# Kernel tuning notes

Hardware: AMD Instinct MI355X
Metric: run time of the kernel (lower is better)

## Reference

```python
import jax, jax.numpy as jnp
import numpy as np

V, E, H = 32000, 512, 512
B, T = 64, 512


def lstm_dir(x, W, U, b, reverse=False):
    """Keras-semantics LSTM over [B,T,D] -> (hs [B,T,H], h_last, c_last).
    Gate order i,f,g,o; sigmoid recurrent activation, tanh activation.
    Inference mode: dropout=0.1 is inactive (Keras applies it only in training)."""
    xz = jnp.einsum('btd,dg->btg', x, W) + b  # precompute input projections [B,T,4H]
    if reverse:
        xz = xz[:, ::-1]
    h0 = jnp.zeros((x.shape[0], U.shape[0]), x.dtype)
    c0 = jnp.zeros_like(h0)

    def step(carry, zt):
        h, c = carry
        z = zt + h @ U
        i, f, g, o = jnp.split(z, 4, axis=-1)
        c = jax.nn.sigmoid(f) * c + jax.nn.sigmoid(i) * jnp.tanh(g)
        h = jax.nn.sigmoid(o) * jnp.tanh(c)
        return (h, c), h

    (h_last, c_last), hs = jax.lax.scan(step, (h0, c0), jnp.swapaxes(xz, 0, 1))
    hs = jnp.swapaxes(hs, 0, 1)  # [B,T,H]
    if reverse:
        hs = hs[:, ::-1]  # Keras Bidirectional re-aligns backward outputs in time
    return hs, h_last, c_last


def setup_inputs() -> dict:
    key = jax.random.key(0)
    ks = jax.random.split(key, 14)
    s = lambda fan_in: 1.0 / np.sqrt(fan_in)
    p = {
        'encoderinput': jax.random.randint(ks[0], (B, T), 0, V, dtype=jnp.int32),
        'emb': jax.random.normal(ks[1], (V, E), jnp.float32) * 0.02,
        # layer 1 (input dim E), forward and backward directions
        'W1f': jax.random.normal(ks[2], (E, 4 * H), jnp.float32) * s(E),
        'U1f': jax.random.normal(ks[3], (H, 4 * H), jnp.float32) * s(H),
        'b1f': jnp.zeros((4 * H,), jnp.float32),
        'W1b': jax.random.normal(ks[4], (E, 4 * H), jnp.float32) * s(E),
        'U1b': jax.random.normal(ks[5], (H, 4 * H), jnp.float32) * s(H),
        'b1b': jnp.zeros((4 * H,), jnp.float32),
        # layer 2 (input dim 2H from bidirectional concat)
        'W2f': jax.random.normal(ks[6], (2 * H, 4 * H), jnp.float32) * s(2 * H),
        'U2f': jax.random.normal(ks[7], (H, 4 * H), jnp.float32) * s(H),
        'b2f': jnp.zeros((4 * H,), jnp.float32),
        'W2b': jax.random.normal(ks[8], (2 * H, 4 * H), jnp.float32) * s(2 * H),
        'U2b': jax.random.normal(ks[9], (H, 4 * H), jnp.float32) * s(H),
        'b2b': jnp.zeros((4 * H,), jnp.float32),
    }
    return p


def reference(encoderinput, emb, W1f, U1f, b1f, W1b, U1b, b1b,
              W2f, U2f, b2f, W2b, U2b, b2b):
    x = emb[encoderinput]  # [B,T,E]
    hf1, _, _ = lstm_dir(x, W1f, U1f, b1f, reverse=False)
    hb1, _, _ = lstm_dir(x, W1b, U1b, b1b, reverse=True)
    l1 = jnp.concatenate([hf1, hb1], axis=-1)  # [B,T,2H]
    hf2, fh, fc = lstm_dir(l1, W2f, U2f, b2f, reverse=False)
    hb2, bh, bc = lstm_dir(l1, W2b, U2b, b2b, reverse=True)
    encoder_output = jnp.concatenate([hf2, hb2], axis=-1)  # [B,T,2H]
    state_h = jnp.concatenate([fh, bh], axis=-1)  # [B,2H]
    state_c = jnp.concatenate([fc, bc], axis=-1)  # [B,2H]
    return (encoder_output, state_h, state_c)
```

## Files before the change

kernel.cpp:

```cpp
#include <hip/hip_runtime.h>
#include <math.h>


#define NBLK_LSTM 256

typedef __attribute__((ext_vector_type(8))) short bf16x8;
typedef __attribute__((ext_vector_type(16))) float f32x16;

__device__ __forceinline__ float bf2f(unsigned short u) {
  return __uint_as_float(((unsigned)u) << 16);
}
__device__ __forceinline__ unsigned short f2bf(float f) {
  unsigned u = __float_as_uint(f);
  unsigned r = (u + 0x7FFFu + ((u >> 16) & 1u)) >> 16;
  return (unsigned short)r;
}
__device__ __forceinline__ float fsigmoid(float x) {
  return 1.0f / (1.0f + __expf(-x));
}
__device__ __forceinline__ float ftanh(float x) {
  return 1.0f - 2.0f / (1.0f + __expf(2.0f * x));
}
__device__ __forceinline__ void gload16(const void* g, void* l) {
  __builtin_amdgcn_global_load_lds(
      (const __attribute__((address_space(1))) unsigned int*)g,
      (__attribute__((address_space(3))) unsigned int*)l, 16, 0, 0);
}

__global__ __launch_bounds__(256) void transpose_u(const float* __restrict__ U,
                                                   float* __restrict__ Ut) {
  __shared__ float tile[32][33];
  int kt = blockIdx.x & 15;
  int ct = blockIdx.x >> 4;
  int k0 = kt * 32, c0 = ct * 32;
  int tx = threadIdx.x & 31, ty = threadIdx.x >> 5;
#pragma unroll
  for (int i = 0; i < 32; i += 8)
    tile[ty + i][tx] = U[(size_t)(k0 + ty + i) * 2048 + c0 + tx];
  __syncthreads();
#pragma unroll
  for (int i = 0; i < 32; i += 8)
    Ut[(size_t)(c0 + ty + i) * 512 + k0 + tx] = tile[tx][ty + i];
}

__global__ __launch_bounds__(256) void build_w_panels(
    const float* __restrict__ W, unsigned short* __restrict__ Wh,
    unsigned short* __restrict__ Wl, int KT) {
  __shared__ float tile[32][33];
  const int tid = threadIdx.x;
  int kt = blockIdx.x % KT;
  int ct = blockIdx.x / KT;
  int k0 = kt * 32, c0 = ct * 32;
  int tx = tid & 31, ty = tid >> 5;
#pragma unroll
  for (int i = 0; i < 32; i += 8)
    tile[ty + i][tx] = W[(size_t)(k0 + ty + i) * 2048 + c0 + tx];
  __syncthreads();
  const int t = tid & 127;
  const int cl = t & 31, g = t >> 5;
  const int c = c0 + cl;
  const int rm = c & 127, nt = c >> 7;
  const int slot = g ^ (rm & 3);
  size_t off = (((size_t)(nt * KT + kt) * 128 + rm) << 5) + slot * 8;
  bf16x8 hh, ll;
#pragma unroll
  for (int e = 0; e < 8; e++) {
    float f = tile[g * 8 + e][cl];
    unsigned short h = f2bf(f);
    hh[e] = (short)h;
    ll[e] = (short)f2bf(f - bf2f(h));
  }
  if (tid < 128) *(bf16x8*)(Wh + off) = hh;
  else           *(bf16x8*)(Wl + off) = ll;
}

__global__ __launch_bounds__(256) void build_a1_panels(
    const int* __restrict__ ids, const float* __restrict__ emb,
    unsigned short* __restrict__ Apan) {
  const int tid = threadIdx.x;
  const int l = tid & 63, wv = tid >> 6;
  const int m = blockIdx.x * 4 + wv;
  const float* src = emb + (size_t)ids[m] * 512 + l * 8;
  float4 v0 = *(const float4*)src;
  float4 v1 = *(const float4*)(src + 4);
  float f[8] = {v0.x, v0.y, v0.z, v0.w, v1.x, v1.y, v1.z, v1.w};
  bf16x8 hh;
#pragma unroll
  for (int e = 0; e < 8; e++) hh[e] = (short)f2bf(f[e]);
  const int rm = m & 127, mt = m >> 7;
  const int kt = l >> 2, g = l & 3;
  const int slot = g ^ (rm & 3);
  *(bf16x8*)(Apan + (((size_t)(mt * 16 + kt) * 128 + rm) << 5) + slot * 8) = hh;
}

template <int KT, int TERMS>
__global__ __launch_bounds__(256) void gemm_panel(
    const unsigned short* __restrict__ Apan,
    const unsigned short* __restrict__ WhF,
    const unsigned short* __restrict__ WlF,
    const unsigned short* __restrict__ WhB,
    const unsigned short* __restrict__ WlB,
    const float* __restrict__ bF, const float* __restrict__ bB,
    unsigned short* __restrict__ CF, unsigned short* __restrict__ CB) {
  __shared__ __align__(16) char lds[2][24576];

  const int tid = threadIdx.x;
  const int half = blockIdx.x >> 12;
  const int inner = blockIdx.x & 4095;
  const int mt = inner & 255;
  const int nt = inner >> 8;
  const int l = tid & 63;
  const int wv = tid >> 6;
  const int wm = wv >> 1, wn = wv & 1;

  const unsigned short* WhP = half ? WhB : WhF;
  const unsigned short* WlP = half ? WlB : WlF;
  const float* bias = half ? bB : bF;
  unsigned short* C = half ? CB : CF;

  const char* aSrc = (const char*)(Apan + (size_t)mt * KT * 4096);
  const char* hSrc = (const char*)(WhP + (size_t)nt * KT * 4096);
  const char* lSrc = (const char*)(WlP + (size_t)nt * KT * 4096);
  const int wvo = wv * 1024;
  const int lo16 = l * 16;

  f32x16 acc[2][2];
#pragma unroll
  for (int rb = 0; rb < 2; rb++)
#pragma unroll
    for (int cb = 0; cb < 2; cb++)
#pragma unroll
      for (int r = 0; r < 16; r++) acc[rb][cb][r] = 0.0f;

  auto STAGE = [&](int buf, int t) {
    const char* ga = aSrc + (size_t)t * 8192 + wvo + lo16;
    const char* gh = hSrc + (size_t)t * 8192 + wvo + lo16;
    char* da = &lds[buf][0] + wvo;
    char* dh = &lds[buf][8192] + wvo;
    gload16(ga, da);
    gload16(ga + 4096, da + 4096);
    gload16(gh, dh);
    gload16(gh + 4096, dh + 4096);
    if (TERMS == 2) {
      const char* gl = lSrc + (size_t)t * 8192 + wvo + lo16;
      char* dl = &lds[buf][16384] + wvo;
      gload16(gl, dl);
      gload16(gl + 4096, dl + 4096);
    }
  };

  STAGE(0, 0);
  asm volatile("s_waitcnt vmcnt(0)" ::: "memory");
  __syncthreads();

  const int aoff0 = (wm * 64 + (l & 31)) * 64;
  const int woff0 = 8192 + (wn * 64 + (l & 31)) * 64;
  const int gbase = l >> 5;
  const int gx = l & 3;

  for (int t = 0; t < KT; t++) {
    if (t + 1 < KT) STAGE((t + 1) & 1, t + 1);
    const char* lb = lds[t & 1];
#pragma unroll
    for (int ks = 0; ks < 2; ks++) {
      const int slot = (((ks << 1) + gbase) ^ gx) << 4;
      bf16x8 a0 = *(const bf16x8*)(lb + aoff0 + slot);
      bf16x8 a1 = *(const bf16x8*)(lb + aoff0 + 2048 + slot);
      bf16x8 h0 = *(const bf16x8*)(lb + woff0 + slot);
      bf16x8 h1 = *(const bf16x8*)(lb + woff0 + 2048 + slot);
      acc[0][0] = __builtin_amdgcn_mfma_f32_32x32x16_bf16(a0, h0, acc[0][0], 0, 0, 0);
      acc[0][1] = __builtin_amdgcn_mfma_f32_32x32x16_bf16(a0, h1, acc[0][1], 0, 0, 0);
      acc[1][0] = __builtin_amdgcn_mfma_f32_32x32x16_bf16(a1, h0, acc[1][0], 0, 0, 0);
      acc[1][1] = __builtin_amdgcn_mfma_f32_32x32x16_bf16(a1, h1, acc[1][1], 0, 0, 0);
      if (TERMS == 2) {
        bf16x8 w0 = *(const bf16x8*)(lb + woff0 + 8192 + slot);
        bf16x8 w1 = *(const bf16x8*)(lb + woff0 + 8192 + 2048 + slot);
        acc[0][0] = __builtin_amdgcn_mfma_f32_32x32x16_bf16(a0, w0, acc[0][0], 0, 0, 0);
        acc[0][1] = __builtin_amdgcn_mfma_f32_32x32x16_bf16(a0, w1, acc[0][1], 0, 0, 0);
        acc[1][0] = __builtin_amdgcn_mfma_f32_32x32x16_bf16(a1, w0, acc[1][0], 0, 0, 0);
        acc[1][1] = __builtin_amdgcn_mfma_f32_32x32x16_bf16(a1, w1, acc[1][1], 0, 0, 0);
      }
    }
    asm volatile("s_waitcnt vmcnt(0)" ::: "memory");
    __syncthreads();
  }

  const int m0 = mt * 128, n0 = nt * 128;
  const float b0 = bias[n0 + wn * 64 + (l & 31)];
  const float b1 = bias[n0 + wn * 64 + 32 + (l & 31)];
#pragma unroll
  for (int rb = 0; rb < 2; rb++) {
    const int rowb = m0 + wm * 64 + rb * 32 + 4 * (l >> 5);
#pragma unroll
    for (int cb = 0; cb < 2; cb++) {
      const int col = n0 + wn * 64 + cb * 32 + (l & 31);
      const float bb = cb ? b1 : b0;
#pragma unroll
      for (int r = 0; r < 16; r++) {
        const int row = rowb + (r & 3) + 8 * (r >> 2);
        C[(size_t)row * 2048 + col] = f2bf(acc[rb][cb][r] + bb);
      }
    }
  }
}

__global__ __launch_bounds__(256, 1) void lstm_fused(
    const unsigned short* __restrict__ xzF,
    const unsigned short* __restrict__ xzB,
    const float* __restrict__ UtF,
    const float* __restrict__ UtB,
    float* __restrict__ outF32,
    unsigned short* __restrict__ outB16,
    float* __restrict__ hbuf,
    float* __restrict__ stateh, float* __restrict__ statec,
    unsigned* __restrict__ bar) {
  __shared__ float p_lds[2][4][32][36];

  const int tid = threadIdx.x;
  const int bid = blockIdx.x;
  const int dir = bid >> 7;
  const int jg  = (bid & 127) >> 1;
  const int bg  = bid & 1;
  const int grp = dir * 2 + bg;

  const unsigned short* xz = dir ? xzB : xzF;
  const float* Ut = dir ? UtB : UtF;
  char* hbuf_c = (char*)hbuf;

  const int l  = tid & 63;
  const int wv = tid >> 6;

  bf16x8 uh8[8], ul8[8];
  {
    const int c = l & 31;
    const size_t gcol = (size_t)((c >> 3) * 512 + jg * 8 + (c & 7));
#pragma unroll
    for (int ks = 0; ks < 8; ks++) {
      const float* src = Ut + gcol * 512 + (wv * 8 + ks) * 16 + ((l >> 5) << 3);
      bf16x8 hh, ll;
#pragma unroll
      for (int e = 0; e < 8; e++) {
        float f = src[e];
        unsigned short us = f2bf(f);
        hh[e] = (short)us;
        ll[e] = (short)f2bf(f - bf2f(us));
      }
      uh8[ks] = hh;
      ul8[ks] = ll;
    }
  }

  const int ub = tid >> 3;
  const int jl = tid & 7;
  const int b  = bg * 32 + ub;
  const int j  = jg * 8 + jl;

  unsigned* leafArr = bar + grp * 128;
  unsigned* arriveLeaf = leafArr + ((jg >> 3) << 4);
  const unsigned* pollLeaf = leafArr + ((l & 7) << 4);

  const unsigned short* xzb = xz + (size_t)b * (512 * 2048) + j;

  float creg = 0.0f;
  float zx0, zx1, zx2, zx3;
  {
    const unsigned short* p = xzb + (size_t)(dir ? 511 : 0) * 2048;
    zx0 = bf2f(p[0]); zx1 = bf2f(p[512]);
    zx2 = bf2f(p[1024]); zx3 = bf2f(p[1536]);
  }

  const int aoff = ((wv * 16 + (l >> 5)) * 32 + (l & 31)) * 16;
  const int poff = jg * 512 + ub * 16 + jl * 2;

  const int colp = dir * 512 + j;
  const int p_kt = colp >> 5, p_g = (colp >> 3) & 3, p_e = colp & 7;

  for (int s = 0; s < 512; s++) {
    const int tt = dir ? (511 - s) : s;

    if (s > 0) {
      {
        const unsigned tgt = 32u * (unsigned)s;
        while (true) {
          unsigned v = __hip_atomic_load(pollLeaf, __ATOMIC_RELAXED,
                                         __HIP_MEMORY_SCOPE_AGENT);
          if (__all((int)(v >= tgt))) break;
          __builtin_amdgcn_s_sleep(1);
        }
      }
      const char* sb = hbuf_c + (size_t)(grp * 2 + (s & 1)) * 65536;
      bf16x8 ahh[8], ahl[8];
#pragma unroll
      for (int ks = 0; ks < 8; ks++) {
        const char* p = sb + aoff + ks * 1024;
        asm volatile("global_load_dwordx4 %0, %1, off sc0 sc1"
                     : "=v"(ahh[ks]) : "v"(p) : "memory");
      }
#pragma unroll
      for (int ks = 0; ks < 8; ks++) {
        const char* p = sb + aoff + ks * 1024 + 32768;
        asm volatile("global_load_dwordx4 %0, %1, off sc0 sc1"
                     : "=v"(ahl[ks]) : "v"(p) : "memory");
      }
      f32x16 acc;
#pragma unroll
      for (int r = 0; r < 16; r++) acc[r] = 0.0f;
      asm volatile("s_waitcnt vmcnt(8)" ::: "memory");
      __builtin_amdgcn_sched_barrier(0);
#pragma unroll
      for (int ks = 0; ks < 8; ks++)
        acc = __builtin_amdgcn_mfma_f32_32x32x16_bf16(ahh[ks], uh8[ks], acc, 0, 0, 0);
      asm volatile("s_waitcnt vmcnt(0)" ::: "memory");
      __builtin_amdgcn_sched_barrier(0);
#pragma unroll
      for (int ks = 0; ks < 8; ks++) {
        acc = __builtin_amdgcn_mfma_f32_32x32x16_bf16(ahl[ks], uh8[ks], acc, 0, 0, 0);
        acc = __builtin_amdgcn_mfma_f32_32x32x16_bf16(ahh[ks], ul8[ks], acc, 0, 0, 0);
      }
#pragma unroll
      for (int r = 0; r < 16; r++) {
        const int row = (r & 3) + 8 * (r >> 2) + 4 * (l >> 5);
        p_lds[s & 1][wv][row][l & 31] = acc[r];
      }
    }
    __syncthreads();

    float h;
    {
      float z0 = zx0, z1 = zx1, z2 = zx2, z3 = zx3;
      if (s > 0) {
#pragma unroll
        for (int w = 0; w < 4; w++) {
          z0 += p_lds[s & 1][w][ub][jl];
          z1 += p_lds[s & 1][w][ub][8 + jl];
          z2 += p_lds[s & 1][w][ub][16 + jl];
          z3 += p_lds[s & 1][w][ub][24 + jl];
        }
      }
      float si = fsigmoid(z0);
      float sf = fsigmoid(z1);
      float tg = ftanh(z2);
      float so = fsigmoid(z3);
      creg = fmaf(sf, creg, si * tg);
      h = so * ftanh(creg);
    }

    const int m = b * 512 + tt;
    if (s < 511) {
      unsigned short hhs = f2bf(h);
      unsigned short hls = f2bf(h - bf2f(hhs));
      char* db = hbuf_c + (size_t)(grp * 2 + ((s & 1) ^ 1)) * 65536;
      char* pj = db + poff;
      unsigned vh = hhs, vl = hls;
      asm volatile("global_store_short %0, %1, off sc0 sc1"
                   :: "v"(pj), "v"(vh) : "memory");
      asm volatile("global_store_short %0, %1, off sc0 sc1"
                   :: "v"(pj + 32768), "v"(vl) : "memory");
      if (outB16) {
        const int rm = m & 127, mt = m >> 7;
        outB16[(((size_t)(mt * 32 + p_kt) * 128 + rm) << 5) +
               (p_g ^ (rm & 3)) * 8 + p_e] = f2bf(h);
      } else {
        outF32[((size_t)m) * 1024 + colp] = h;
      }
      asm volatile("s_waitcnt vmcnt(0)" ::: "memory");
      if ((tid & 63) == 0)
        __hip_atomic_fetch_add(arriveLeaf, 1u, __ATOMIC_RELAXED,
                               __HIP_MEMORY_SCOPE_AGENT);
      {
        const int tn = dir ? (510 - s) : (s + 1);
        const unsigned short* p = xzb + (size_t)tn * 2048;
        zx0 = bf2f(p[0]); zx1 = bf2f(p[512]);
        zx2 = bf2f(p[1024]); zx3 = bf2f(p[1536]);
      }
    } else {
      if (outB16) {
        const int rm = m & 127, mt = m >> 7;
        outB16[(((size_t)(mt * 32 + p_kt) * 128 + rm) << 5) +
               (p_g ^ (rm & 3)) * 8 + p_e] = f2bf(h);
      } else {
        outF32[((size_t)m) * 1024 + colp] = h;
      }
      if (stateh != nullptr) {
        stateh[b * 1024 + colp] = h;
        statec[b * 1024 + colp] = creg;
      }
    }
  }
}

extern "C" void kernel_launch(void* const* d_in, const int* in_sizes, int n_in,
                              void* d_out, int out_size, void* d_ws, size_t ws_size,
                              hipStream_t stream) {
  const int*   ids = (const int*)d_in[0];
  const float* emb = (const float*)d_in[1];
  const float* W1f = (const float*)d_in[2];
  const float* U1f = (const float*)d_in[3];
  const float* b1f = (const float*)d_in[4];
  const float* W1b = (const float*)d_in[5];
  const float* U1b = (const float*)d_in[6];
  const float* b1b = (const float*)d_in[7];
  const float* W2f = (const float*)d_in[8];
  const float* U2f = (const float*)d_in[9];
  const float* b2f = (const float*)d_in[10];
  const float* W2b = (const float*)d_in[11];
  const float* U2b = (const float*)d_in[12];
  const float* b2b = (const float*)d_in[13];
  float* out = (float*)d_out;

  char* ws = (char*)d_ws;
  unsigned short* xzF = (unsigned short*)(ws + 0ull);
  unsigned short* xzB = (unsigned short*)(ws + 134217728ull);
  float* Ut1f = (float*)(ws + 268435456ull);
  float* Ut1b = Ut1f + 1048576;
  float* Ut2f = Ut1b + 1048576;
  float* Ut2b = Ut2f + 1048576;
  float* hbuf = (float*)(ws + 285212672ull);
  unsigned* bar = (unsigned*)(ws + 285736960ull);

  char* outc = (char*)d_out;
  unsigned short* l1pan = (unsigned short*)outc;
  unsigned short* A1pan = (unsigned short*)(outc + 67108864ull);
  unsigned short* Wh1f = (unsigned short*)(outc + 100663296ull);
  unsigned short* Wl1f = (unsigned short*)(outc + 102760448ull);
  unsigned short* Wh1b = (unsigned short*)(outc + 104857600ull);
  unsigned short* Wl1b = (unsigned short*)(outc + 106954752ull);
  unsigned short* Wh2f = (unsigned short*)(outc + 109051904ull);
  unsigned short* Wl2f = (unsigned short*)(outc + 113246208ull);
  unsigned short* Wh2b = (unsigned short*)(outc + 117440512ull);
  unsigned short* Wl2b = (unsigned short*)(outc + 121634816ull);

  transpose_u<<<1024, 256, 0, stream>>>(U1f, Ut1f);
  transpose_u<<<1024, 256, 0, stream>>>(U1b, Ut1b);
  transpose_u<<<1024, 256, 0, stream>>>(U2f, Ut2f);
  transpose_u<<<1024, 256, 0, stream>>>(U2b, Ut2b);
  build_w_panels<<<1024, 256, 0, stream>>>(W1f, Wh1f, Wl1f, 16);
  build_w_panels<<<1024, 256, 0, stream>>>(W1b, Wh1b, Wl1b, 16);
  build_w_panels<<<2048, 256, 0, stream>>>(W2f, Wh2f, Wl2f, 32);
  build_w_panels<<<2048, 256, 0, stream>>>(W2b, Wh2b, Wl2b, 32);
  build_a1_panels<<<8192, 256, 0, stream>>>(ids, emb, A1pan);

  gemm_panel<16, 1><<<8192, 256, 0, stream>>>(A1pan, Wh1f, Wl1f, Wh1b, Wl1b,
                                              b1f, b1b, xzF, xzB);
  hipMemsetAsync(bar, 0, 4096, stream);
  lstm_fused<<<NBLK_LSTM, 256, 0, stream>>>(xzF, xzB, Ut1f, Ut1b,
                                            nullptr, l1pan, hbuf,
                                            nullptr, nullptr, bar);
  gemm_panel<32, 2><<<8192, 256, 0, stream>>>(l1pan, Wh2f, Wl2f, Wh2b, Wl2b,
                                              b2f, b2b, xzF, xzB);
  hipMemsetAsync(bar, 0, 4096, stream);
  lstm_fused<<<NBLK_LSTM, 256, 0, stream>>>(xzF, xzB, Ut2f, Ut2b,
                                            out, nullptr, hbuf,
                                            out + 33554432, out + 33619968, bar);
}
```

Baseline: 4.076 ms.

## Merge prep kernel launches, fold barrier reset into GEMM, signal arrival earlier

The four U transposes are merged into one launch, and the W panel builds are merged per layer. The two memsets that clear the barrier are replaced by block 0 of the preceding GEMM zeroing the counters. In the LSTM step, each wave now signals arrival right after writing its h exchange buffer, before the output store, which shortens the critical path of the cross-block barrier on every timestep. The aim is to cut launch overhead and the per-step sync latency. Zeroing the barrier inside the GEMM depends on the GEMM finishing before the LSTM launch, which stream order guarantees.

```diff
diff --git a/kernel.cpp b/kernel.cpp
--- a/kernel.cpp
+++ b/kernel.cpp
@@ -27,11 +27,18 @@
       (__attribute__((address_space(3))) unsigned int*)l, 16, 0, 0);
 }
 
-__global__ __launch_bounds__(256) void transpose_u(const float* __restrict__ U,
-                                                   float* __restrict__ Ut) {
+__global__ __launch_bounds__(256) void transpose_u4(
+    const float* __restrict__ U0, const float* __restrict__ U1,
+    const float* __restrict__ U2, const float* __restrict__ U3,
+    float* __restrict__ T0, float* __restrict__ T1,
+    float* __restrict__ T2, float* __restrict__ T3) {
   __shared__ float tile[32][33];
-  int kt = blockIdx.x & 15;
-  int ct = blockIdx.x >> 4;
+  const int which = blockIdx.x >> 10;
+  const int inner = blockIdx.x & 1023;
+  const float* U = which == 0 ? U0 : which == 1 ? U1 : which == 2 ? U2 : U3;
+  float* Ut      = which == 0 ? T0 : which == 1 ? T1 : which == 2 ? T2 : T3;
+  int kt = inner & 15;
+  int ct = inner >> 4;
   int k0 = kt * 32, c0 = ct * 32;
   int tx = threadIdx.x & 31, ty = threadIdx.x >> 5;
 #pragma unroll
@@ -43,13 +50,22 @@
     Ut[(size_t)(c0 + ty + i) * 512 + k0 + tx] = tile[tx][ty + i];
 }
 
+template <int KT>
 __global__ __launch_bounds__(256) void build_w_panels(
-    const float* __restrict__ W, unsigned short* __restrict__ Wh,
-    unsigned short* __restrict__ Wl, int KT) {
+    const float* __restrict__ WF, unsigned short* __restrict__ WhFp,
+    unsigned short* __restrict__ WlFp,
+    const float* __restrict__ WB, unsigned short* __restrict__ WhBp,
+    unsigned short* __restrict__ WlBp) {
   __shared__ float tile[32][33];
   const int tid = threadIdx.x;
-  int kt = blockIdx.x % KT;
-  int ct = blockIdx.x / KT;
+  const int nInner = KT * 64;
+  const int half = blockIdx.x / nInner;
+  const int inner = blockIdx.x % nInner;
+  const float* W = half ? WB : WF;
+  unsigned short* Wh = half ? WhBp : WhFp;
+  unsigned short* Wl = half ? WlBp : WlFp;
+  int kt = inner % KT;
+  int ct = inner / KT;
   int k0 = kt * 32, c0 = ct * 32;
   int tx = tid & 31, ty = tid >> 5;
 #pragma unroll
@@ -101,10 +117,15 @@
     const unsigned short* __restrict__ WhB,
     const unsigned short* __restrict__ WlB,
     const float* __restrict__ bF, const float* __restrict__ bB,
-    unsigned short* __restrict__ CF, unsigned short* __restrict__ CB) {
+    unsigned short* __restrict__ CF, unsigned short* __restrict__ CB,
+    unsigned* __restrict__ barz) {
   __shared__ __align__(16) char lds[2][24576];
 
   const int tid = threadIdx.x;
+  if (blockIdx.x == 0 && tid < 128) {
+    uint4 z = {0u, 0u, 0u, 0u};
+    ((uint4*)barz)[tid] = z;
+  }
   const int half = blockIdx.x >> 12;
   const int inner = blockIdx.x & 4095;
   const int mt = inner & 255;
@@ -356,6 +377,10 @@
                    :: "v"(pj), "v"(vh) : "memory");
       asm volatile("global_store_short %0, %1, off sc0 sc1"
                    :: "v"(pj + 32768), "v"(vl) : "memory");
+      asm volatile("s_waitcnt vmcnt(0)" ::: "memory");
+      if ((tid & 63) == 0)
+        __hip_atomic_fetch_add(arriveLeaf, 1u, __ATOMIC_RELAXED,
+                               __HIP_MEMORY_SCOPE_AGENT);
       if (outB16) {
         const int rm = m & 127, mt = m >> 7;
         outB16[(((size_t)(mt * 32 + p_kt) * 128 + rm) << 5) +
@@ -363,10 +388,6 @@
       } else {
         outF32[((size_t)m) * 1024 + colp] = h;
       }
-      asm volatile("s_waitcnt vmcnt(0)" ::: "memory");
-      if ((tid & 63) == 0)
-        __hip_atomic_fetch_add(arriveLeaf, 1u, __ATOMIC_RELAXED,
-                               __HIP_MEMORY_SCOPE_AGENT);
       {
         const int tn = dir ? (510 - s) : (s + 1);
         const unsigned short* p = xzb + (size_t)tn * 2048;
@@ -430,25 +451,19 @@
   unsigned short* Wh2b = (unsigned short*)(outc + 117440512ull);
   unsigned short* Wl2b = (unsigned short*)(outc + 121634816ull);
 
-  transpose_u<<<1024, 256, 0, stream>>>(U1f, Ut1f);
-  transpose_u<<<1024, 256, 0, stream>>>(U1b, Ut1b);
-  transpose_u<<<1024, 256, 0, stream>>>(U2f, Ut2f);
-  transpose_u<<<1024, 256, 0, stream>>>(U2b, Ut2b);
-  build_w_panels<<<1024, 256, 0, stream>>>(W1f, Wh1f, Wl1f, 16);
-  build_w_panels<<<1024, 256, 0, stream>>>(W1b, Wh1b, Wl1b, 16);
-  build_w_panels<<<2048, 256, 0, stream>>>(W2f, Wh2f, Wl2f, 32);
-  build_w_panels<<<2048, 256, 0, stream>>>(W2b, Wh2b, Wl2b, 32);
+  transpose_u4<<<4096, 256, 0, stream>>>(U1f, U1b, U2f, U2b,
+                                         Ut1f, Ut1b, Ut2f, Ut2b);
+  build_w_panels<16><<<2048, 256, 0, stream>>>(W1f, Wh1f, Wl1f, W1b, Wh1b, Wl1b);
+  build_w_panels<32><<<4096, 256, 0, stream>>>(W2f, Wh2f, Wl2f, W2b, Wh2b, Wl2b);
   build_a1_panels<<<8192, 256, 0, stream>>>(ids, emb, A1pan);
 
   gemm_panel<16, 1><<<8192, 256, 0, stream>>>(A1pan, Wh1f, Wl1f, Wh1b, Wl1b,
-                                              b1f, b1b, xzF, xzB);
-  hipMemsetAsync(bar, 0, 4096, stream);
+                                              b1f, b1b, xzF, xzB, bar);
   lstm_fused<<<NBLK_LSTM, 256, 0, stream>>>(xzF, xzB, Ut1f, Ut1b,
                                             nullptr, l1pan, hbuf,
                                             nullptr, nullptr, bar);
   gemm_panel<32, 2><<<8192, 256, 0, stream>>>(l1pan, Wh2f, Wl2f, Wh2b, Wl2b,
-                                              b2f, b2b, xzF, xzB);
-  hipMemsetAsync(bar, 0, 4096, stream);
+                                              b2f, b2b, xzF, xzB, bar);
   lstm_fused<<<NBLK_LSTM, 256, 0, stream>>>(xzF, xzB, Ut2f, Ut2b,
                                             out, nullptr, hbuf,
                                             out + 33554432, out + 33619968, bar);
```

Result: no change. 4.016 ms (-1.5%).
